# Performance work log

Measured on AMD Instinct MI355X. Metric: run time of the kernel, lower is better.

## Reference

```python
import jax, jax.numpy as jnp
import numpy as np

NEG = -1e32
EPS_LN = 1e-5

def _layer_norm(x, w, b):
    mu = jnp.mean(x, axis=-1, keepdims=True)
    var = jnp.mean((x - mu) ** 2, axis=-1, keepdims=True)
    return (x - mu) / jnp.sqrt(var + EPS_LN) * w + b

def setup_inputs() -> dict:
    key = jax.random.key(0)
    ks = jax.random.split(key, 10)
    B, S, D, H, F = 2, 2048, 1024, 16, 4096
    s = 0.02
    return {
        "query": jax.random.normal(ks[0], (B, S, D), jnp.float32),
        "key": jax.random.normal(ks[1], (B, S, D), jnp.float32),
        "values": jax.random.normal(ks[2], (B, S, D), jnp.float32),
        "Wk": jax.random.normal(ks[3], (D, D), jnp.float32) * s,
        "bk": jnp.zeros((D,), jnp.float32),
        "Wv": jax.random.normal(ks[4], (D, D), jnp.float32) * s,
        "bv": jnp.zeros((D,), jnp.float32),
        "Wo": jax.random.normal(ks[5], (D, D), jnp.float32) * s,
        "bo": jnp.zeros((D,), jnp.float32),
        "gammas": jax.random.normal(ks[6], (H, 1, 1), jnp.float32),
        "ln1_w": jnp.ones((D,), jnp.float32),
        "ln1_b": jnp.zeros((D,), jnp.float32),
        "W1": jax.random.normal(ks[7], (F, D), jnp.float32) * s,
        "b1": jnp.zeros((F,), jnp.float32),
        "W2": jax.random.normal(ks[8], (D, F), jnp.float32) * s,
        "b2": jnp.zeros((D,), jnp.float32),
        "ln2_w": jnp.ones((D,), jnp.float32),
        "ln2_b": jnp.zeros((D,), jnp.float32),
        "mask": 1,
    }

def _forward(query, key, values, Wk, bk, Wv, bv, Wo, bo, gammas,
             ln1_w, ln1_b, W1, b1, W2, b2, ln2_w, ln2_b, mask):
    B, S, D = query.shape
    H = gammas.shape[0]
    dk = D // H
    # kq_same=True: q and k both use k_linear
    def proj(x, W, b):
        return (x @ W.T + b).reshape(B, S, H, dk).transpose(0, 2, 1, 3)  # bhsd
    q = proj(query, Wk, bk)
    k = proj(key, Wk, bk)
    v = proj(values, Wv, bv)

    scores = jnp.einsum("bhqd,bhkd->bhqk", q, k) / np.sqrt(dk).astype(np.float32)
    # src_mask: np.triu(ones, k=mask)==0 -> allowed where j <= i + mask - 1
    allow = jnp.tril(jnp.ones((S, S), bool), k=mask - 1)[None, None]  # (1,1,S,S)

    # --- distance decay (no_grad block in torch) ---
    scores_ = jax.nn.softmax(jnp.where(allow, scores, NEG), axis=-1)
    scores_ = scores_ * allow.astype(scores_.dtype)
    distcum = jnp.cumsum(scores_, axis=-1)
    disttotal = jnp.sum(scores_, axis=-1, keepdims=True)
    idx = jnp.arange(S)
    position_effect = jnp.abs(idx[:, None] - idx[None, :]).astype(jnp.float32)[None, None]
    dist_scores = jnp.sqrt(jnp.clip((disttotal - distcum) * position_effect, 0.0, None))
    gamma = -jax.nn.softplus(gammas)[None]  # (1,H,1,1)
    total_effect = jnp.clip(jnp.exp(dist_scores * gamma), 1e-5, 1e5)
    total_effect = jax.lax.stop_gradient(total_effect)
    # ---

    scores = scores * total_effect
    scores = jnp.where(allow, scores, NEG)
    attn = jax.nn.softmax(scores, axis=-1)
    out = jnp.einsum("bhqk,bhkd->bhqd", attn, v)
    concat = out.transpose(0, 2, 1, 3).reshape(B, S, D)
    query2 = concat @ Wo.T + bo

    x = _layer_norm(query + query2, ln1_w, ln1_b)
    ff = jax.nn.relu(x @ W1.T + b1) @ W2.T + b2
    x = _layer_norm(x + ff, ln2_w, ln2_b)
    return x

def reference(query, key, values, Wk, bk, Wv, bv, Wo, bo, gammas,
              ln1_w, ln1_b, W1, b1, W2, b2, ln2_w, ln2_b, mask):
    return _forward(query, key, values, Wk, bk, Wv, bv, Wo, bo, gammas,
                    ln1_w, ln1_b, W1, b1, W2, b2, ln2_w, ln2_b, mask)
```

## Files before the change

### kernel.cpp

```cpp
#include <hip/hip_runtime.h>
#include <hip/hip_bf16.h>

#define B_   2
#define S_   2048
#define D_   1024
#define H_   16
#define DK_  64
#define F_   4096
#define M_   (B_*S_)
#define PD   72

typedef __attribute__((ext_vector_type(8))) short short8;
typedef __attribute__((ext_vector_type(4))) float f32x4;

__device__ __forceinline__ float bf2f(unsigned short s) { return __uint_as_float(((unsigned int)s) << 16); }
__device__ __forceinline__ unsigned short f2bf(float f) {
    unsigned int u = __float_as_uint(f);
    u += 0x7fffu + ((u >> 16) & 1u);
    return (unsigned short)(u >> 16);
}

__device__ __forceinline__ bool probe_f32(const unsigned int* p) {
    return *p == 0x3F800000u;
}
__device__ __forceinline__ float ld1e(const void* p, size_t idx, bool f32) {
    return f32 ? ((const float*)p)[idx] : bf2f(((const unsigned short*)p)[idx]);
}
__device__ __forceinline__ void st1e(void* p, size_t idx, bool f32, float v) {
    if (f32) ((float*)p)[idx] = v;
    else     ((unsigned short*)p)[idx] = f2bf(v);
}

__device__ __forceinline__ void async16(void* lds, const void* g) {
    __builtin_amdgcn_global_load_lds(
        (const __attribute__((address_space(1))) void*)g,
        (__attribute__((address_space(3))) void*)lds, 16, 0, 0);
}

__device__ __forceinline__ unsigned int cvt_pk_bf16(float a, float b) {
    unsigned int r;
    asm("v_cvt_pk_bf16_f32 %0, %1, %2" : "=v"(r) : "v"(a), "v"(b));
    return r;
}

template <bool IS_MAX>
__device__ __forceinline__ float block_reduce(float val, float* buf, int tid) {
    buf[tid] = val;
    __syncthreads();
    #pragma unroll
    for (int off = 128; off > 0; off >>= 1) {
        if (tid < off) {
            float o = buf[tid + off];
            buf[tid] = IS_MAX ? fmaxf(buf[tid], o) : (buf[tid] + o);
        }
        __syncthreads();
    }
    float r = buf[0];
    __syncthreads();
    return r;
}

__global__ __launch_bounds__(256) void cvt_all(
    const void* __restrict__ W1, const void* __restrict__ W2,
    const void* __restrict__ Wk, const void* __restrict__ Wv,
    const void* __restrict__ Wo,
    const void* __restrict__ Qi, const void* __restrict__ Ki,
    const void* __restrict__ Vi,
    unsigned short* __restrict__ W1b, unsigned short* __restrict__ W2b,
    unsigned short* __restrict__ Wkb, unsigned short* __restrict__ Wvb,
    unsigned short* __restrict__ Wob,
    unsigned short* __restrict__ qcb, unsigned short* __restrict__ kcb,
    unsigned short* __restrict__ vcb,
    const unsigned int* __restrict__ probe)
{
    const bool p32 = probe_f32(probe);
    const int blk = blockIdx.x;
    const void* src;
    unsigned short* dst;
    int off;
    if (blk < 2048)      { src = W1; dst = W1b; off = blk; }
    else if (blk < 4096) { src = W2; dst = W2b; off = blk - 2048; }
    else if (blk < 4608) { src = Wk; dst = Wkb; off = blk - 4096; }
    else if (blk < 5120) { src = Wv; dst = Wvb; off = blk - 4608; }
    else if (blk < 5632) { src = Wo; dst = Wob; off = blk - 5120; }
    else if (blk < 7680) { if (!p32) return; src = Qi; dst = qcb; off = blk - 5632; }
    else if (blk < 9728) { if (!p32) return; src = Ki; dst = kcb; off = blk - 7680; }
    else                 { if (!p32) return; src = Vi; dst = vcb; off = blk - 9728; }
    const int i8 = (off * 256 + threadIdx.x) * 8;
    if (p32) {
        const float4 a = *(const float4*)((const float*)src + i8);
        const float4 b = *(const float4*)((const float*)src + i8 + 4);
        short8 o;
        o[0] = (short)f2bf(a.x); o[1] = (short)f2bf(a.y);
        o[2] = (short)f2bf(a.z); o[3] = (short)f2bf(a.w);
        o[4] = (short)f2bf(b.x); o[5] = (short)f2bf(b.y);
        o[6] = (short)f2bf(b.z); o[7] = (short)f2bf(b.w);
        *(short8*)(dst + i8) = o;
    } else {
        *(uint4*)(dst + i8) = *(const uint4*)((const unsigned short*)src + i8);
    }
}

template <int RELU, int AEXT, int CEXT>
__device__ __forceinline__ void gemm_body(
    const void* __restrict__ A,
    const unsigned short* __restrict__ W,
    const void* __restrict__ bias,
    void* __restrict__ C,
    int M, int N, int K, bool p32, int bx, int by)
{
    __shared__ unsigned short As[2][128 * 32];
    __shared__ unsigned short Ws[2][128 * 32];

    const bool a32 = AEXT && p32;
    const bool c32 = CEXT && p32;

    const int tid = threadIdx.x;
    const int lane = tid & 63;
    const int w = tid >> 6;
    const int wr = w >> 1;
    const int wc = w & 1;
    const int col16 = lane & 15;
    const int quad = lane >> 4;

    const int m0 = by * 128;
    const int n0 = bx * 128;

    const int c0 = tid, c1 = 256 + tid;
    const int r0 = c0 >> 2, kc0 = (c0 & 3) * 8;
    const int r1 = c1 >> 2, kc1 = (c1 & 3) * 8;

    f32x4 acc[4][4];
    #pragma unroll
    for (int mt = 0; mt < 4; mt++)
        #pragma unroll
        for (int nt = 0; nt < 4; nt++)
            acc[mt][nt] = (f32x4){0.f, 0.f, 0.f, 0.f};

    auto stage = [&](int bb, int k0) {
        async16(&Ws[bb][c0 * 8], W + (size_t)(n0 + r0) * K + k0 + kc0);
        async16(&Ws[bb][c1 * 8], W + (size_t)(n0 + r1) * K + k0 + kc1);
        if (a32) {
            const float* a0 = (const float*)A + (size_t)(m0 + r0) * K + k0 + kc0;
            const float* a1 = (const float*)A + (size_t)(m0 + r1) * K + k0 + kc1;
            const float4 x0 = *(const float4*)a0, y0 = *(const float4*)(a0 + 4);
            const float4 x1 = *(const float4*)a1, y1 = *(const float4*)(a1 + 4);
            short8 s0, s1;
            s0[0] = (short)f2bf(x0.x); s0[1] = (short)f2bf(x0.y);
            s0[2] = (short)f2bf(x0.z); s0[3] = (short)f2bf(x0.w);
            s0[4] = (short)f2bf(y0.x); s0[5] = (short)f2bf(y0.y);
            s0[6] = (short)f2bf(y0.z); s0[7] = (short)f2bf(y0.w);
            s1[0] = (short)f2bf(x1.x); s1[1] = (short)f2bf(x1.y);
            s1[2] = (short)f2bf(x1.z); s1[3] = (short)f2bf(x1.w);
            s1[4] = (short)f2bf(y1.x); s1[5] = (short)f2bf(y1.y);
            s1[6] = (short)f2bf(y1.z); s1[7] = (short)f2bf(y1.w);
            *(short8*)&As[bb][c0 * 8] = s0;
            *(short8*)&As[bb][c1 * 8] = s1;
        } else {
            const unsigned short* Ab = (const unsigned short*)A;
            async16(&As[bb][c0 * 8], Ab + (size_t)(m0 + r0) * K + k0 + kc0);
            async16(&As[bb][c1 * 8], Ab + (size_t)(m0 + r1) * K + k0 + kc1);
        }
    };

    stage(0, 0);
    __syncthreads();
    int cur = 0;
    for (int k0 = 0; k0 < K; k0 += 32) {
        const int nxt = cur ^ 1;
        if (k0 + 32 < K) stage(nxt, k0 + 32);

        short8 av[4], bv[4];
        #pragma unroll
        for (int mt = 0; mt < 4; mt++)
            av[mt] = *(const short8*)&As[cur][(wr * 64 + mt * 16 + col16) * 32 + quad * 8];
        #pragma unroll
        for (int nt = 0; nt < 4; nt++)
            bv[nt] = *(const short8*)&Ws[cur][(wc * 64 + nt * 16 + col16) * 32 + quad * 8];
        #pragma unroll
        for (int mt = 0; mt < 4; mt++)
            #pragma unroll
            for (int nt = 0; nt < 4; nt++)
                acc[mt][nt] = __builtin_amdgcn_mfma_f32_16x16x32_bf16(
                    av[mt], bv[nt], acc[mt][nt], 0, 0, 0);
        __syncthreads();
        cur = nxt;
    }

    #pragma unroll
    for (int mt = 0; mt < 4; mt++) {
        const int row = m0 + wr * 64 + mt * 16 + quad * 4;
        #pragma unroll
        for (int nt = 0; nt < 4; nt++) {
            const int col = n0 + wc * 64 + nt * 16 + col16;
            const float bb = ld1e(bias, col, p32);
            #pragma unroll
            for (int r = 0; r < 4; r++) {
                float v = acc[mt][nt][r] + bb;
                if (RELU) v = fmaxf(v, 0.f);
                st1e(C, (size_t)(row + r) * N + col, c32, v);
            }
        }
    }
}

template <int RELU, int AEXT, int CEXT>
__global__ __launch_bounds__(256) void gemm_mf(
    const void* __restrict__ A,
    const unsigned short* __restrict__ W,
    const void* __restrict__ bias,
    void* __restrict__ C,
    int M, int N, int K,
    const unsigned int* __restrict__ probe)
{
    gemm_body<RELU, AEXT, CEXT>(A, W, bias, C, M, N, K, probe_f32(probe),
                                blockIdx.x, blockIdx.y);
}

template <int RELU, int CEXT>
__global__ __launch_bounds__(512) void gemm_sk(
    const unsigned short* __restrict__ A,
    const unsigned short* __restrict__ W,
    const void* __restrict__ bias,
    void* __restrict__ C,
    int M, int N, int K,
    const unsigned int* __restrict__ probe)
{
    __shared__ unsigned short SS[2][2][2][128 * 32];
    float* const R = (float*)&SS[0][0][0][0];

    const bool p32 = probe_f32(probe);
    const bool c32 = CEXT && p32;

    const int tid = threadIdx.x;
    const int g = tid >> 8;
    const int tl = tid & 255;
    const int lane = tl & 63;
    const int w = tl >> 6;
    const int wr = w >> 1;
    const int wc = w & 1;
    const int col16 = lane & 15;
    const int quad = lane >> 4;

    const int m0 = blockIdx.y * 128;
    const int n0 = blockIdx.x * 128;

    const int c0 = tl, c1 = 256 + tl;
    const int r0 = c0 >> 2, kc0 = (c0 & 3) * 8;
    const int r1 = c1 >> 2, kc1 = (c1 & 3) * 8;

    const int Kh = K >> 1;
    const int kbeg = g * Kh;

    f32x4 acc[4][4];
    #pragma unroll
    for (int mt = 0; mt < 4; mt++)
        #pragma unroll
        for (int nt = 0; nt < 4; nt++)
            acc[mt][nt] = (f32x4){0.f, 0.f, 0.f, 0.f};

    auto stage = [&](int bb, int k0) {
        async16(&SS[g][bb][1][c0 * 8], W + (size_t)(n0 + r0) * K + k0 + kc0);
        async16(&SS[g][bb][1][c1 * 8], W + (size_t)(n0 + r1) * K + k0 + kc1);
        async16(&SS[g][bb][0][c0 * 8], A + (size_t)(m0 + r0) * K + k0 + kc0);
        async16(&SS[g][bb][0][c1 * 8], A + (size_t)(m0 + r1) * K + k0 + kc1);
    };

    stage(0, kbeg);
    __syncthreads();
    int cur = 0;
    for (int kk = 0; kk < Kh; kk += 32) {
        const int nxt = cur ^ 1;
        if (kk + 32 < Kh) stage(nxt, kbeg + kk + 32);

        short8 av[4], bv[4];
        #pragma unroll
        for (int mt = 0; mt < 4; mt++)
            av[mt] = *(const short8*)&SS[g][cur][0][(wr * 64 + mt * 16 + col16) * 32 + quad * 8];
        #pragma unroll
        for (int nt = 0; nt < 4; nt++)
            bv[nt] = *(const short8*)&SS[g][cur][1][(wc * 64 + nt * 16 + col16) * 32 + quad * 8];
        #pragma unroll
        for (int mt = 0; mt < 4; mt++)
            #pragma unroll
            for (int nt = 0; nt < 4; nt++)
                acc[mt][nt] = __builtin_amdgcn_mfma_f32_16x16x32_bf16(
                    av[mt], bv[nt], acc[mt][nt], 0, 0, 0);
        __syncthreads();
        cur = nxt;
    }

    __syncthreads();
    if (g == 1) {
        #pragma unroll
        for (int mt = 0; mt < 4; mt++)
            #pragma unroll
            for (int nt = 0; nt < 4; nt++) {
                const int lrow = wr * 64 + mt * 16 + quad * 4;
                const int lcol = wc * 64 + nt * 16 + col16;
                #pragma unroll
                for (int r = 0; r < 4; r++)
                    R[(lrow + r) * 128 + lcol] = acc[mt][nt][r];
            }
    }
    __syncthreads();
    if (g == 0) {
        #pragma unroll
        for (int mt = 0; mt < 4; mt++) {
            const int lrow = wr * 64 + mt * 16 + quad * 4;
            const int row = m0 + lrow;
            #pragma unroll
            for (int nt = 0; nt < 4; nt++) {
                const int lcol = wc * 64 + nt * 16 + col16;
                const int col = n0 + lcol;
                const float bb = ld1e(bias, col, p32);
                #pragma unroll
                for (int r = 0; r < 4; r++) {
                    float v = acc[mt][nt][r] + R[(lrow + r) * 128 + lcol] + bb;
                    if (RELU) v = fmaxf(v, 0.f);
                    st1e(C, (size_t)(row + r) * N + col, c32, v);
                }
            }
        }
    }
}

__global__ __launch_bounds__(256) void gemm_proj(
    const void* __restrict__ q_orig, const void* __restrict__ k_orig,
    const void* __restrict__ v_orig,
    const unsigned short* __restrict__ qcb, const unsigned short* __restrict__ kcb,
    const unsigned short* __restrict__ vcb,
    const unsigned short* __restrict__ Wkb, const unsigned short* __restrict__ Wvb,
    const void* __restrict__ bk, const void* __restrict__ bv,
    unsigned short* __restrict__ qw, unsigned short* __restrict__ kw,
    unsigned short* __restrict__ vw,
    const unsigned int* __restrict__ probe)
{
    const bool p32 = probe_f32(probe);
    const int z = blockIdx.z;
    const unsigned short* W = (z == 2) ? Wvb : Wkb;
    const void* bias = (z == 2) ? bv : bk;
    void* C = (z == 0) ? (void*)qw : (z == 1) ? (void*)kw : (void*)vw;
    if (z == 2 && p32 && vcb == nullptr) {
        gemm_body<0, 1, 0>(v_orig, W, bias, C, M_, D_, D_, p32,
                           blockIdx.x, blockIdx.y);
    } else {
        const void* A = (z == 0) ? (p32 ? (const void*)qcb : q_orig)
                      : (z == 1) ? (p32 ? (const void*)kcb : k_orig)
                                 : (p32 ? (const void*)vcb : v_orig);
        gemm_body<0, 0, 0>(A, W, bias, C, M_, D_, D_, p32,
                           blockIdx.x, blockIdx.y);
    }
}

__global__ __launch_bounds__(256) void vtrans(
    const unsigned short* __restrict__ vw,
    unsigned short* __restrict__ vtg)
{
    __shared__ unsigned short T[64 * PD];
    const int tid = threadIdx.x;
    const int bid = blockIdx.x;
    const int bh = bid & 31;
    const int kt = bid >> 5;
    const int h = bh & 15, b = bh >> 4;
    #pragma unroll
    for (int cc = 0; cc < 2; cc++) {
        const int c = tid + cc * 256;
        const int key = c >> 3, dc = c & 7;
        const uint4 u = *(const uint4*)(vw + (size_t)(b * S_ + kt * 64 + key) * D_ + h * 64 + dc * 8);
        unsigned short* dst = &T[(dc * 8) * PD + key];
        dst[0 * PD] = (unsigned short)(u.x & 0xffff);
        dst[1 * PD] = (unsigned short)(u.x >> 16);
        dst[2 * PD] = (unsigned short)(u.y & 0xffff);
        dst[3 * PD] = (unsigned short)(u.y >> 16);
        dst[4 * PD] = (unsigned short)(u.z & 0xffff);
        dst[5 * PD] = (unsigned short)(u.z >> 16);
        dst[6 * PD] = (unsigned short)(u.w & 0xffff);
        dst[7 * PD] = (unsigned short)(u.w >> 16);
    }
    __syncthreads();
    #pragma unroll
    for (int cc = 0; cc < 2; cc++) {
        const int c = tid + cc * 256;
        const int d = c >> 3, kc = c & 7;
        const uint4 u = *(const uint4*)&T[d * PD + kc * 8];
        *(uint4*)(vtg + ((size_t)bh * 64 + d) * S_ + kt * 64 + kc * 8) = u;
    }
}

__global__ __launch_bounds__(256) void attn_mfma(
    const unsigned short* __restrict__ qw,
    const unsigned short* __restrict__ kw,
    const unsigned short* __restrict__ vtg,
    const void* __restrict__ gam,
    const int* __restrict__ maskp,
    unsigned short* __restrict__ outc,
    const unsigned int* __restrict__ probe)
{
    __shared__ unsigned short Qs[64 * PD];
    __shared__ unsigned short Ks[64 * PD];
    __shared__ unsigned short Vt[64 * PD];
    __shared__ float ctS[64 * 33];
    __shared__ float rT1S[64];
    unsigned int* const Pu = (unsigned int*)Qs;

    const bool p32 = probe_f32(probe);
    const int tid = threadIdx.x;
    const int lane = tid & 63;
    const int w = tid >> 6;
    const int col16 = lane & 15;
    const int quad = lane >> 4;
    const int bid = blockIdx.x;
    const int qt = 31 - (bid >> 5);
    const int bh = bid & 31;
    const int h = bh & 15;
    const int b = bh >> 4;
    const int i0 = qt * 64;

    const int mask = *maskp;
    long long nje = (long long)i0 + 63 + (long long)mask;
    int njmax = (nje > S_) ? S_ : (int)nje;
    if (njmax < 1) njmax = 1;
    const int ntiles = (njmax + 63) >> 6;
    long long fm = (long long)i0 + (long long)mask - 64;
    int nfull = 0;
    if (fm >= 0) {
        long long v = (fm >> 6) + 1;
        nfull = (v > ntiles) ? ntiles : (int)v;
    }

    const float L2E = 1.44269504088896f;
    const float gval = ld1e(gam, h, p32);
    const float sp = (gval > 20.f) ? gval : log1pf(__expf(gval));
    const float g2 = -sp * L2E;
    const float SC2 = 0.125f * L2E;

    const int myrow = i0 + w * 16 + col16;
    const int limq = myrow + mask - quad * 4;

    #pragma unroll
    for (int cc = 0; cc < 2; cc++) {
        const int c = tid + cc * 256;
        const int row = c >> 3, dc = c & 7;
        const uint4 u = *(const uint4*)(qw + (size_t)(b * S_ + i0 + row) * D_ + h * 64 + dc * 8);
        *(uint4*)&Qs[row * PD + dc * 8] = u;
    }
    __syncthreads();

    short8 avq[2];
    #pragma unroll
    for (int ks = 0; ks < 2; ks++)
        avq[ks] = *(const short8*)&Qs[(w * 16 + col16) * PD + ks * 32 + quad * 8];

    for (int t = 0; t < ntiles; t++) {
        const int j0 = t * 64;
        __syncthreads();
        #pragma unroll
        for (int cc = 0; cc < 2; cc++) {
            const int c = tid + cc * 256;
            const int row = c >> 3, dc = c & 7;
            const uint4 u = *(const uint4*)(kw + (size_t)(b * S_ + j0 + row) * D_ + h * 64 + dc * 8);
            *(uint4*)&Ks[row * PD + dc * 8] = u;
        }
        __syncthreads();

        f32x4 acc[4];
        #pragma unroll
        for (int nt = 0; nt < 4; nt++) acc[nt] = (f32x4){0.f, 0.f, 0.f, 0.f};
        #pragma unroll
        for (int ks = 0; ks < 2; ks++)
            #pragma unroll
            for (int nt = 0; nt < 4; nt++) {
                const short8 kv = *(const short8*)&Ks[(nt * 16 + col16) * PD + ks * 32 + quad * 8];
                acc[nt] = __builtin_amdgcn_mfma_f32_16x16x32_bf16(kv, avq[ks], acc[nt], 0, 0, 0);
            }

        if (t >= nfull) {
            #pragma unroll
            for (int nt = 0; nt < 4; nt++) {
                const int Ln = limq - j0 - nt * 16;
                #pragma unroll
                for (int r = 0; r < 4; r++)
                    acc[nt][r] = (r < Ln) ? acc[nt][r] : -3.0e38f;
            }
        }

        float cs = 0.f;
        #pragma unroll
        for (int nt = 0; nt < 4; nt++)
            #pragma unroll
            for (int r = 0; r < 4; r++)
                cs += __builtin_amdgcn_exp2f(acc[nt][r] * SC2);
        cs += __shfl_xor(cs, 16, 64);
        cs += __shfl_xor(cs, 32, 64);

        if (lane < 16)
            ctS[(w * 16 + lane) * 33 + t] = cs;
    }

    __syncthreads();
    if (lane < 16) {
        const int row = w * 16 + lane;
        float runv = 0.f;
        for (int t = 0; t < ntiles; t++) {
            const float e = ctS[row * 33 + t];
            ctS[row * 33 + t] = runv;
            runv += e;
        }
        rT1S[row] = 1.0f / runv;
    }
    __syncthreads();

    const float rT1 = rT1S[w * 16 + col16];

    float l2 = 0.f;
    f32x4 O[4];
    #pragma unroll
    for (int nt = 0; nt < 4; nt++) O[nt] = (f32x4){0.f, 0.f, 0.f, 0.f};

    for (int t = 0; t < ntiles; t++) {
        const int j0 = t * 64;
        __syncthreads();
        #pragma unroll
        for (int cc = 0; cc < 2; cc++) {
            const int c = tid + cc * 256;
            const int row = c >> 3, dc = c & 7;
            const uint4 u = *(const uint4*)(kw + (size_t)(b * S_ + j0 + row) * D_ + h * 64 + dc * 8);
            *(uint4*)&Ks[row * PD + dc * 8] = u;
        }
        #pragma unroll
        for (int cc = 0; cc < 2; cc++) {
            const int c = tid + cc * 256;
            const int d = c >> 3, kc = c & 7;
            const uint4 u = *(const uint4*)(vtg + ((size_t)bh * 64 + d) * S_ + j0 + kc * 8);
            *(uint4*)&Vt[d * PD + kc * 8] = u;
        }
        __syncthreads();

        f32x4 acc[4];
        #pragma unroll
        for (int nt = 0; nt < 4; nt++) acc[nt] = (f32x4){0.f, 0.f, 0.f, 0.f};
        #pragma unroll
        for (int ks = 0; ks < 2; ks++)
            #pragma unroll
            for (int nt = 0; nt < 4; nt++) {
                const short8 kv = *(const short8*)&Ks[(nt * 16 + col16) * PD + ks * 32 + quad * 8];
                acc[nt] = __builtin_amdgcn_mfma_f32_16x16x32_bf16(kv, avq[ks], acc[nt], 0, 0, 0);
            }

        if (t >= nfull) {
            #pragma unroll
            for (int nt = 0; nt < 4; nt++) {
                const int Ln = limq - j0 - nt * 16;
                #pragma unroll
                for (int r = 0; r < 4; r++)
                    acc[nt][r] = (r < Ln) ? acc[nt][r] : -3.0e38f;
            }
        }

        float s2v[4][4], loc[4][4], run4[4];
        #pragma unroll
        for (int nt = 0; nt < 4; nt++) {
            float rr = 0.f;
            #pragma unroll
            for (int r = 0; r < 4; r++) {
                const float s2 = acc[nt][r] * SC2;
                s2v[nt][r] = s2;
                rr += __builtin_amdgcn_exp2f(s2);
                loc[nt][r] = rr;
            }
            run4[nt] = rr;
        }
        float excl[4], tot[4];
        #pragma unroll
        for (int nt = 0; nt < 4; nt++) {
            float v = run4[nt];
            const float u1 = __shfl_up(v, 16, 64); if (quad >= 1) v += u1;
            const float u2 = __shfl_up(v, 32, 64); if (quad >= 2) v += u2;
            excl[nt] = v - run4[nt];
            tot[nt] = __shfl(v, col16 + 48, 64);
        }

        const float pref = ctS[(w * 16 + col16) * 33 + t];
        float Cb = pref;
        #pragma unroll
        for (int nt = 0; nt < 4; nt++) {
            const float CeR = (Cb + excl[nt]) * rT1;
            const float d0f = (float)(myrow - j0 - nt * 16 - quad * 4);
            float p4[4];
            #pragma unroll
            for (int r = 0; r < 4; r++) {
                const float cumn = __builtin_fmaf(loc[nt][r], rT1, CeR);
                const float rem = fmaxf(1.f - cumn, 0.f);
                const float pe = fabsf(d0f - (float)r);
                const float te = fmaxf(
                    __builtin_amdgcn_exp2f(g2 * __builtin_amdgcn_sqrtf(rem * pe)), 1e-5f);
                const float tv = s2v[nt][r] * te;
                p4[r] = __builtin_amdgcn_exp2f(tv);
                l2 += p4[r];
            }
            uint2 pk;
            pk.x = cvt_pk_bf16(p4[0], p4[1]);
            pk.y = cvt_pk_bf16(p4[2], p4[3]);
            *(uint2*)&Pu[(w * 16 + col16) * 36 + nt * 8 + quad * 2] = pk;
            Cb += tot[nt];
        }

        const short8 pa0 = *(const short8*)&Pu[(w * 16 + col16) * 36 + 0 * 16 + quad * 4];
        const short8 pa1 = *(const short8*)&Pu[(w * 16 + col16) * 36 + 1 * 16 + quad * 4];
        #pragma unroll
        for (int nt = 0; nt < 4; nt++) {
            const short8 bv0 = *(const short8*)&Vt[(nt * 16 + col16) * PD + 0 * 32 + quad * 8];
            const short8 bv1 = *(const short8*)&Vt[(nt * 16 + col16) * PD + 1 * 32 + quad * 8];
            O[nt] = __builtin_amdgcn_mfma_f32_16x16x32_bf16(pa0, bv0, O[nt], 0, 0, 0);
            O[nt] = __builtin_amdgcn_mfma_f32_16x16x32_bf16(pa1, bv1, O[nt], 0, 0, 0);
        }
    }

    l2 += __shfl_xor(l2, 16, 64);
    l2 += __shfl_xor(l2, 32, 64);
    const float rl2 = 1.0f / l2;
    float rl2O[4];
    #pragma unroll
    for (int r = 0; r < 4; r++) rl2O[r] = __shfl(rl2, quad * 4 + r, 64);
    #pragma unroll
    for (int nt = 0; nt < 4; nt++)
        #pragma unroll
        for (int r = 0; r < 4; r++)
            outc[(size_t)(b * S_ + i0 + w * 16 + quad * 4 + r) * D_ + h * 64 + nt * 16 + col16] =
                f2bf(O[nt][r] * rl2O[r]);
}

__global__ __launch_bounds__(256) void ln_fused(
    const void* __restrict__ A,
    const void* __restrict__ Bq,
    const void* __restrict__ w,
    const void* __restrict__ bias,
    void* __restrict__ out,
    const unsigned int* __restrict__ probe, int aext, int bext, int oext)
{
    __shared__ float xs[D_];
    __shared__ float red[256];
    const bool p32 = probe_f32(probe);
    const bool a32 = aext && p32;
    const bool b32 = bext && p32;
    const bool o32 = oext && p32;

    const int tid = threadIdx.x;
    const size_t row = (size_t)blockIdx.x * D_;

    float lsum = 0.f;
    #pragma unroll
    for (int qq = 0; qq < 4; qq++) {
        const int j = tid + qq * 256;
        const float x = ld1e(A, row + j, a32) + ld1e(Bq, row + j, b32);
        xs[j] = x;
        lsum += x;
    }
    const float mu = block_reduce<false>(lsum, red, tid) * (1.0f / D_);

    float lv = 0.f;
    #pragma unroll
    for (int qq = 0; qq < 4; qq++) {
        const int j = tid + qq * 256;
        const float dd = xs[j] - mu;
        lv += dd * dd;
    }
    const float var = block_reduce<false>(lv, red, tid) * (1.0f / D_);
    const float rs = rsqrtf(var + 1e-5f);

    #pragma unroll
    for (int qq = 0; qq < 4; qq++) {
        const int j = tid + qq * 256;
        const float o = (xs[j] - mu) * rs * ld1e(w, j, p32) + ld1e(bias, j, p32);
        st1e(out, row + j, o32, o);
    }
}

extern "C" void kernel_launch(void* const* d_in, const int* in_sizes, int n_in,
                              void* d_out, int out_size, void* d_ws, size_t ws_size,
                              hipStream_t stream)
{
    (void)in_sizes; (void)n_in; (void)out_size;

    const void* query  = d_in[0];
    const void* key_   = d_in[1];
    const void* values = d_in[2];
    const void* Wk     = d_in[3];
    const void* bk     = d_in[4];
    const void* Wv     = d_in[5];
    const void* bv     = d_in[6];
    const void* Wo     = d_in[7];
    const void* bo     = d_in[8];
    const void* gammas = d_in[9];
    const void* ln1w   = d_in[10];
    const void* ln1b   = d_in[11];
    const void* W1     = d_in[12];
    const void* b1     = d_in[13];
    const void* W2     = d_in[14];
    const void* b2     = d_in[15];
    const void* ln2w   = d_in[16];
    const void* ln2b   = d_in[17];
    const int*  maskp  = (const int*)d_in[18];
    const unsigned int* probe = (const unsigned int*)ln1w;

    char* ws = (char*)d_ws;
    const size_t MiB = 1024 * 1024;
    unsigned short* W1b = (unsigned short*)(ws + 0 * MiB);
    unsigned short* W2b = (unsigned short*)(ws + 8 * MiB);
    unsigned short* Wkb = (unsigned short*)(ws + 16 * MiB);
    unsigned short* Wvb = (unsigned short*)(ws + 18 * MiB);
    unsigned short* Wob = (unsigned short*)(ws + 20 * MiB);
    unsigned short* qw  = (unsigned short*)(ws + 22 * MiB);
    unsigned short* kw  = (unsigned short*)(ws + 30 * MiB);
    unsigned short* vw  = (unsigned short*)(ws + 38 * MiB);
    unsigned short* cw  = (unsigned short*)(ws + 46 * MiB);
    unsigned short* vtg = (unsigned short*)(ws + 54 * MiB);
    unsigned short* x1  = (unsigned short*)(ws + 22 * MiB);
    unsigned short* fh  = (unsigned short*)(ws + 30 * MiB);
    unsigned short* qc  = (unsigned short*)(ws + 46 * MiB);
    unsigned short* kc  = (unsigned short*)(ws + 54 * MiB);
    unsigned short* vc  = (ws_size >= (size_t)70 * MiB)
                          ? (unsigned short*)(ws + 62 * MiB) : nullptr;

    const dim3 blk(256);
    const dim3 blk5(512);
    const int cvtgrid = vc ? 11776 : 9728;
    cvt_all<<<dim3(cvtgrid), blk, 0, stream>>>(
        W1, W2, Wk, Wv, Wo, query, key_, values,
        W1b, W2b, Wkb, Wvb, Wob, qc, kc, vc, probe);
    gemm_proj<<<dim3(D_ / 128, M_ / 128, 3), blk, 0, stream>>>(
        query, key_, values, qc, kc, vc, Wkb, Wvb, bk, bv, qw, kw, vw, probe);
    vtrans<<<dim3(1024), blk, 0, stream>>>(vw, vtg);
    attn_mfma<<<dim3(B_ * H_ * (S_ / 64)), blk, 0, stream>>>(
        qw, kw, vtg, gammas, maskp, cw, probe);
    gemm_sk<0, 0><<<dim3(D_ / 128, M_ / 128), blk5, 0, stream>>>(
        cw, Wob, bo, x1, M_, D_, D_, probe);
    ln_fused<<<dim3(M_), blk, 0, stream>>>(query, x1, ln1w, ln1b, x1, probe, 1, 0, 0);
    gemm_mf<1, 0, 0><<<dim3(F_ / 128, M_ / 128), blk, 0, stream>>>(
        x1, W1b, b1, fh, M_, F_, D_, probe);
    gemm_sk<0, 1><<<dim3(D_ / 128, M_ / 128), blk5, 0, stream>>>(
        fh, W2b, b2, d_out, M_, D_, F_, probe);
    ln_fused<<<dim3(M_), blk, 0, stream>>>(x1, d_out, ln2w, ln2b, d_out, probe, 0, 1, 1);
}
```

Baseline: 453.0 us.

## Split-K gemm_sk four ways and drop per-tile prefix buffer in attention

The split-K GEMM used for the output and second FFN projections now runs 1024-thread blocks with four K-groups instead of two, reducing partial sums through LDS in two stages. The attention kernel no longer stores per-tile row sums in a shared prefix array. It accumulates the row total in one register and carries a running prefix across tiles in the second pass, which removes the LDS scan and two barriers. The GEMM change raises per-block LDS use and register pressure and adds extra reduction barriers, which may lower occupancy.

```diff
diff --git a/kernel.cpp b/kernel.cpp
--- a/kernel.cpp
+++ b/kernel.cpp
@@ -218,7 +218,7 @@
 }
 
 template <int RELU, int CEXT>
-__global__ __launch_bounds__(512) void gemm_sk(
+__global__ __launch_bounds__(1024) void gemm_sk(
     const unsigned short* __restrict__ A,
     const unsigned short* __restrict__ W,
     const void* __restrict__ bias,
@@ -226,8 +226,9 @@
     int M, int N, int K,
     const unsigned int* __restrict__ probe)
 {
-    __shared__ unsigned short SS[2][2][2][128 * 32];
-    float* const R = (float*)&SS[0][0][0][0];
+    __shared__ unsigned short SS[4][2][2][128 * 32];
+    float* const R0 = (float*)&SS[0][0][0][0];
+    float* const R1 = (float*)&SS[2][0][0][0];
 
     const bool p32 = probe_f32(probe);
     const bool c32 = CEXT && p32;
@@ -249,8 +250,8 @@
     const int r0 = c0 >> 2, kc0 = (c0 & 3) * 8;
     const int r1 = c1 >> 2, kc1 = (c1 & 3) * 8;
 
-    const int Kh = K >> 1;
-    const int kbeg = g * Kh;
+    const int Kq = K >> 2;
+    const int kbeg = g * Kq;
 
     f32x4 acc[4][4];
     #pragma unroll
@@ -269,9 +270,9 @@
     stage(0, kbeg);
     __syncthreads();
     int cur = 0;
-    for (int kk = 0; kk < Kh; kk += 32) {
+    for (int kk = 0; kk < Kq; kk += 32) {
         const int nxt = cur ^ 1;
-        if (kk + 32 < Kh) stage(nxt, kbeg + kk + 32);
+        if (kk + 32 < Kq) stage(nxt, kbeg + kk + 32);
 
         short8 av[4], bv[4];
         #pragma unroll
@@ -290,8 +291,8 @@
         cur = nxt;
     }
 
-    __syncthreads();
-    if (g == 1) {
+    if (g == 1 || g == 3) {
+        float* R = (g == 1) ? R0 : R1;
         #pragma unroll
         for (int mt = 0; mt < 4; mt++)
             #pragma unroll
@@ -304,6 +305,33 @@
             }
     }
     __syncthreads();
+    if (g == 0 || g == 2) {
+        const float* R = (g == 0) ? R0 : R1;
+        #pragma unroll
+        for (int mt = 0; mt < 4; mt++)
+            #pragma unroll
+            for (int nt = 0; nt < 4; nt++) {
+                const int lrow = wr * 64 + mt * 16 + quad * 4;
+                const int lcol = wc * 64 + nt * 16 + col16;
+                #pragma unroll
+                for (int r = 0; r < 4; r++)
+                    acc[mt][nt][r] += R[(lrow + r) * 128 + lcol];
+            }
+    }
+    __syncthreads();
+    if (g == 2) {
+        #pragma unroll
+        for (int mt = 0; mt < 4; mt++)
+            #pragma unroll
+            for (int nt = 0; nt < 4; nt++) {
+                const int lrow = wr * 64 + mt * 16 + quad * 4;
+                const int lcol = wc * 64 + nt * 16 + col16;
+                #pragma unroll
+                for (int r = 0; r < 4; r++)
+                    R0[(lrow + r) * 128 + lcol] = acc[mt][nt][r];
+            }
+    }
+    __syncthreads();
     if (g == 0) {
         #pragma unroll
         for (int mt = 0; mt < 4; mt++) {
@@ -316,7 +344,7 @@
                 const float bb = ld1e(bias, col, p32);
                 #pragma unroll
                 for (int r = 0; r < 4; r++) {
-                    float v = acc[mt][nt][r] + R[(lrow + r) * 128 + lcol] + bb;
+                    float v = acc[mt][nt][r] + R0[(lrow + r) * 128 + lcol] + bb;
                     if (RELU) v = fmaxf(v, 0.f);
                     st1e(C, (size_t)(row + r) * N + col, c32, v);
                 }
@@ -400,8 +428,6 @@
     __shared__ unsigned short Qs[64 * PD];
     __shared__ unsigned short Ks[64 * PD];
     __shared__ unsigned short Vt[64 * PD];
-    __shared__ float ctS[64 * 33];
-    __shared__ float rT1S[64];
     unsigned int* const Pu = (unsigned int*)Qs;
 
     const bool p32 = probe_f32(probe);
@@ -452,6 +478,7 @@
     for (int ks = 0; ks < 2; ks++)
         avq[ks] = *(const short8*)&Qs[(w * 16 + col16) * PD + ks * 32 + quad * 8];
 
+    float T1l = 0.f;
     for (int t = 0; t < ntiles; t++) {
         const int j0 = t * 64;
         __syncthreads();
@@ -485,35 +512,18 @@
             }
         }
 
-        float cs = 0.f;
         #pragma unroll
         for (int nt = 0; nt < 4; nt++)
             #pragma unroll
             for (int r = 0; r < 4; r++)
-                cs += __builtin_amdgcn_exp2f(acc[nt][r] * SC2);
-        cs += __shfl_xor(cs, 16, 64);
-        cs += __shfl_xor(cs, 32, 64);
-
-        if (lane < 16)
-            ctS[(w * 16 + lane) * 33 + t] = cs;
-    }
-
-    __syncthreads();
-    if (lane < 16) {
-        const int row = w * 16 + lane;
-        float runv = 0.f;
-        for (int t = 0; t < ntiles; t++) {
-            const float e = ctS[row * 33 + t];
-            ctS[row * 33 + t] = runv;
-            runv += e;
-        }
-        rT1S[row] = 1.0f / runv;
-    }
-    __syncthreads();
-
-    const float rT1 = rT1S[w * 16 + col16];
+                T1l += __builtin_amdgcn_exp2f(acc[nt][r] * SC2);
+    }
+    T1l += __shfl_xor(T1l, 16, 64);
+    T1l += __shfl_xor(T1l, 32, 64);
+    const float rT1 = 1.0f / T1l;
 
     float l2 = 0.f;
+    float Cb_run = 0.f;
     f32x4 O[4];
     #pragma unroll
     for (int nt = 0; nt < 4; nt++) O[nt] = (f32x4){0.f, 0.f, 0.f, 0.f};
@@ -581,8 +591,7 @@
             tot[nt] = __shfl(v, col16 + 48, 64);
         }
 
-        const float pref = ctS[(w * 16 + col16) * 33 + t];
-        float Cb = pref;
+        float Cb = Cb_run;
         #pragma unroll
         for (int nt = 0; nt < 4; nt++) {
             const float CeR = (Cb + excl[nt]) * rT1;
@@ -605,6 +614,7 @@
             *(uint2*)&Pu[(w * 16 + col16) * 36 + nt * 8 + quad * 2] = pk;
             Cb += tot[nt];
         }
+        Cb_run = Cb;
 
         const short8 pa0 = *(const short8*)&Pu[(w * 16 + col16) * 36 + 0 * 16 + quad * 4];
         const short8 pa1 = *(const short8*)&Pu[(w * 16 + col16) * 36 + 1 * 16 + quad * 4];
@@ -724,7 +734,7 @@
                           ? (unsigned short*)(ws + 62 * MiB) : nullptr;
 
     const dim3 blk(256);
-    const dim3 blk5(512);
+    const dim3 blk10(1024);
     const int cvtgrid = vc ? 11776 : 9728;
     cvt_all<<<dim3(cvtgrid), blk, 0, stream>>>(
         W1, W2, Wk, Wv, Wo, query, key_, values,
@@ -734,12 +744,12 @@
     vtrans<<<dim3(1024), blk, 0, stream>>>(vw, vtg);
     attn_mfma<<<dim3(B_ * H_ * (S_ / 64)), blk, 0, stream>>>(
         qw, kw, vtg, gammas, maskp, cw, probe);
-    gemm_sk<0, 0><<<dim3(D_ / 128, M_ / 128), blk5, 0, stream>>>(
+    gemm_sk<0, 0><<<dim3(D_ / 128, M_ / 128), blk10, 0, stream>>>(
         cw, Wob, bo, x1, M_, D_, D_, probe);
     ln_fused<<<dim3(M_), blk, 0, stream>>>(query, x1, ln1w, ln1b, x1, probe, 1, 0, 0);
     gemm_mf<1, 0, 0><<<dim3(F_ / 128, M_ / 128), blk, 0, stream>>>(
         x1, W1b, b1, fh, M_, F_, D_, probe);
-    gemm_sk<0, 1><<<dim3(D_ / 128, M_ / 128), blk5, 0, stream>>>(
+    gemm_sk<0, 1><<<dim3(D_ / 128, M_ / 128), blk10, 0, stream>>>(
         fh, W2b, b2, d_out, M_, D_, F_, probe);
     ln_fused<<<dim3(M_), blk, 0, stream>>>(x1, d_out, ln2w, ln2b, d_out, probe, 0, 1, 1);
 }
```

Result: no change. 456.1 us (+0.7%).
